# Kernel tuning notes

Measured on AMD Instinct MI355X. Metric: run time of the kernel, lower is better.

## Reference

```python
import jax, jax.numpy as jnp
import numpy as np

LN_EPS = 1e-6

def hsigmoid(v):
    # HSigmoid with bias=3, divisor=6: clamp((v+3)/6, 0, 1)
    return jnp.clip((v + 3.0) / 6.0, 0.0, 1.0)

def setup_inputs() -> dict:
    key = jax.random.key(0)
    ks = jax.random.split(key, 10)
    b, c, h, w = 8, 512, 64, 64
    s = lambda fan: 1.0 / np.sqrt(fan)
    return {
        "x": jax.random.normal(ks[0], (b, c, h, w), jnp.float32),
        "w_b1": jax.random.normal(ks[1], (c // 2, c), jnp.float32) * s(c),
        "b_b1": jax.random.normal(ks[2], (c // 2,), jnp.float32) * 0.01,
        "w_b2": jax.random.normal(ks[3], (c, c // 2), jnp.float32) * s(c // 2),
        "b_b2": jax.random.normal(ks[4], (c,), jnp.float32) * 0.01,
        "w_conv1": jax.random.normal(ks[5], (1, c), jnp.float32) * s(c),
        "ln_g": jnp.ones((c,), jnp.float32),
        "ln_b": jnp.zeros((c,), jnp.float32),
        "sk_w1": jax.random.normal(ks[6], (c // 2, c), jnp.float32) * s(c),
        "sk_w2": jax.random.normal(ks[7], (c, c // 2), jnp.float32) * s(c // 2),
        "res_w": jax.random.normal(ks[8], (c, c), jnp.float32) * s(c),
    }

def reference(x, w_b1, b_b1, w_b2, b_b2, w_conv1, ln_g, ln_b, sk_w1, sk_w2, res_w):
    b, c, h, w = x.shape
    # --- channel attention: GAP -> 1x1 conv+ReLU -> 1x1 conv+HSigmoid -> LN over c ---
    g = x.mean(axis=(2, 3))                                  # (b, c)
    ca = jax.nn.relu(g @ w_b1.T + b_b1)                      # (b, c/2)
    ca = hsigmoid(ca @ w_b2.T + b_b2)                        # (b, c)
    mu = ca.mean(axis=-1, keepdims=True)
    var = ca.var(axis=-1, keepdims=True)
    ca = (ca - mu) / jnp.sqrt(var + LN_EPS) * ln_g + ln_b    # LayerNorm over channels
    channel_attn = ca[:, :, None, None]                      # (b, c, 1, 1)
    # --- spatial attention: 1x1 conv (c->1, no bias) + HSigmoid ---
    spatial_attn = hsigmoid(jnp.einsum('bchw,c->bhw', x, w_conv1[0]))[:, None]  # (b,1,h,w)
    # --- parallel attention: torch float // 2 == floor((a+b)/2) ---
    par_attn = jnp.floor((spatial_attn + channel_attn) / 2.0)  # (b, c, h, w)
    # --- sequence attention: bmm outer product (b,c,1)x(b,1,hw) ---
    seq_attn = channel_attn * spatial_attn                     # (b, c, h, w)
    # --- SK module: GAP(sum) -> conv+ReLU -> conv+ReLU -> softmax over c ---
    u = (seq_attn + par_attn).mean(axis=(2, 3))                # (b, c)
    u = jax.nn.relu(u @ sk_w1.T)
    u = jax.nn.relu(u @ sk_w2.T)
    a = jax.nn.softmax(u, axis=1)[:, :, None, None]            # (b, c, 1, 1)
    selected_attn = seq_attn * a + par_attn * (1.0 - a)        # (b, c, h, w)
    # --- self attention: spatial sum + 1x1 residual conv ---
    self_attn = selected_attn.sum(axis=(2, 3))[:, :, None, None] \
        + jnp.einsum('bchw,oc->bohw', x, res_w)                # (b, c, h, w)
    return x * selected_attn + self_attn
```

## Files before the change

### kernel.cpp

```cpp
#include <hip/hip_runtime.h>
#include <stdint.h>

#define HW 4096
#define NC 512
#define NB 8

typedef __attribute__((ext_vector_type(8))) short short8;
typedef __attribute__((ext_vector_type(4))) float f32x4;

__device__ __forceinline__ unsigned short f2bf(float f) {
  unsigned int u = __builtin_bit_cast(unsigned int, f);
  unsigned int r = (u + 0x7FFFu + ((u >> 16) & 1u)) >> 16;
  return (unsigned short)r;
}
__device__ __forceinline__ float hsig(float v) {
  return fminf(fmaxf((v + 3.0f) * (1.0f / 6.0f), 0.0f), 1.0f);
}

__device__ __forceinline__ void gload16(const void* g, void* l) {
  __builtin_amdgcn_global_load_lds(
      (const __attribute__((address_space(1))) unsigned int*)g,
      (__attribute__((address_space(3))) unsigned int*)l, 16, 0, 0);
}

__device__ __forceinline__ float wave_reduce(float p) {
#pragma unroll
  for (int m = 1; m < 64; m <<= 1) p += __shfl_xor(p, m);
  return p;
}

__device__ __forceinline__ float block_reduce_sum16(float v, volatile float* red) {
  int t = threadIdx.x;
#pragma unroll
  for (int m = 1; m < 64; m <<= 1) v += __shfl_xor(v, m);
  if ((t & 63) == 0) red[t >> 6] = v;
  __syncthreads();
  v = 0.f;
#pragma unroll
  for (int i = 0; i < 16; i++) v += red[i];
  __syncthreads();
  return v;
}
__device__ __forceinline__ float block_reduce_max16(float v, volatile float* red) {
  int t = threadIdx.x;
#pragma unroll
  for (int m = 1; m < 64; m <<= 1) v = fmaxf(v, __shfl_xor(v, m));
  if ((t & 63) == 0) red[t >> 6] = v;
  __syncthreads();
  v = red[0];
#pragma unroll
  for (int i = 1; i < 16; i++) v = fmaxf(v, red[i]);
  __syncthreads();
  return v;
}

__global__ __launch_bounds__(256) void k1_stats_transpose(
    const float* __restrict__ x, const float* __restrict__ w_conv1,
    const float* __restrict__ res_w,
    float* __restrict__ g_sum, float* __restrict__ spat,
    unsigned short* __restrict__ xTS, unsigned short* __restrict__ wbfS) {
  __shared__ float sp_lds[16][64];
  __shared__ unsigned short t_lds[64 * 72];
  const int t = threadIdx.x;
  const int b = blockIdx.z;
  const int c0 = blockIdx.y * 64;
  const int h0 = blockIdx.x * 64;
  const int cg = t >> 4;
  const int hg = t & 15;

  float vv[4][4];
  float wc[4];
  const float* xb = x + ((size_t)(b * NC + c0 + cg * 4) * HW) + h0 + hg * 4;
#pragma unroll
  for (int i = 0; i < 4; i++) {
    float4 v = *(const float4*)(xb + (size_t)i * HW);
    vv[i][0] = v.x; vv[i][1] = v.y; vv[i][2] = v.z; vv[i][3] = v.w;
    wc[i] = w_conv1[c0 + cg * 4 + i];
  }
#pragma unroll
  for (int i = 0; i < 4; i++) {
    float s = vv[i][0] + vv[i][1] + vv[i][2] + vv[i][3];
    s += __shfl_xor(s, 1); s += __shfl_xor(s, 2);
    s += __shfl_xor(s, 4); s += __shfl_xor(s, 8);
    if (hg == 0) atomicAdd(&g_sum[b * NC + c0 + cg * 4 + i], s);
  }
  {
    float4 sp;
    sp.x = vv[0][0] * wc[0] + vv[1][0] * wc[1] + vv[2][0] * wc[2] + vv[3][0] * wc[3];
    sp.y = vv[0][1] * wc[0] + vv[1][1] * wc[1] + vv[2][1] * wc[2] + vv[3][1] * wc[3];
    sp.z = vv[0][2] * wc[0] + vv[1][2] * wc[1] + vv[2][2] * wc[2] + vv[3][2] * wc[3];
    sp.w = vv[0][3] * wc[0] + vv[1][3] * wc[1] + vv[2][3] * wc[2] + vv[3][3] * wc[3];
    *(float4*)&sp_lds[cg][hg * 4] = sp;
  }
#pragma unroll
  for (int j = 0; j < 4; j++) {
    ushort4 u;
    u.x = f2bf(vv[0][j]); u.y = f2bf(vv[1][j]);
    u.z = f2bf(vv[2][j]); u.w = f2bf(vv[3][j]);
    *(ushort4*)&t_lds[(hg * 4 + j) * 72 + cg * 4] = u;
  }
  __syncthreads();
  if (t < 64) {
    float s = 0.f;
#pragma unroll
    for (int i = 0; i < 16; i++) s += sp_lds[i][t];
    atomicAdd(&spat[b * HW + h0 + t], s);
  }
  const int w = t >> 6, l = t & 63;
#pragma unroll
  for (int ff = w; ff < 8; ff += 4) {
    const int fr = ff >> 1, fk = ff & 1;
    short8 v = *(const short8*)&t_lds[(fr * 16 + (l & 15)) * 72 + (fk * 4 + (l >> 4)) * 8];
    size_t tile = (size_t)(b * 256 + (h0 >> 4) + fr) * 16 + (c0 >> 5) + fk;
    *(short8*)(xTS + tile * 512 + l * 8) = v;
  }
  if (b == 0 && t < 64) {
    const int q = blockIdx.y * 64 + blockIdx.x;
    float4 a = *(const float4*)(res_w + (size_t)q * 512 + t * 8);
    float4 c2 = *(const float4*)(res_w + (size_t)q * 512 + t * 8 + 4);
    short8 v;
    v[0] = (short)f2bf(a.x); v[1] = (short)f2bf(a.y);
    v[2] = (short)f2bf(a.z); v[3] = (short)f2bf(a.w);
    v[4] = (short)f2bf(c2.x); v[5] = (short)f2bf(c2.y);
    v[6] = (short)f2bf(c2.z); v[7] = (short)f2bf(c2.w);
    const int lq = (q & 15) + ((t & 3) << 4);
    *(short8*)(wbfS + ((size_t)(q >> 4) * 16 + (t >> 2)) * 512 + lq * 8) = v;
  }
}

__global__ __launch_bounds__(1024) void k2_front(
    const float* __restrict__ g_sum, const float* __restrict__ spat,
    const float* __restrict__ w_b1, const float* __restrict__ b_b1,
    const float* __restrict__ w_b2, const float* __restrict__ b_b2,
    const float* __restrict__ ln_g, const float* __restrict__ ln_b,
    float* __restrict__ s_out, float* __restrict__ Ssum,
    float* __restrict__ t_arr) {
  __shared__ float ca1_l[256];
  __shared__ float ca2_l[512];
  __shared__ float red[16];
  const int b = blockIdx.x, t = threadIdx.x;
  const int w = t >> 6, l = t & 63;

  {
    float4 v = ((const float4*)(spat + (size_t)b * HW))[t];
    float4 os;
    os.x = hsig(v.x); os.y = hsig(v.y); os.z = hsig(v.z); os.w = hsig(v.w);
    ((float4*)(s_out + (size_t)b * HW))[t] = os;
    float Ss = block_reduce_sum16(os.x + os.y + os.z + os.w, red);
    if (t == 0) Ssum[b] = Ss;
  }

  float ga[8];
  {
    const float4 g0 = *(const float4*)(g_sum + b * NC + l * 8);
    const float4 g1 = *(const float4*)(g_sum + b * NC + l * 8 + 4);
    ga[0] = g0.x; ga[1] = g0.y; ga[2] = g0.z; ga[3] = g0.w;
    ga[4] = g1.x; ga[5] = g1.y; ga[6] = g1.z; ga[7] = g1.w;
  }
#pragma unroll
  for (int jj = 0; jj < 4; jj++) {
    float pr[4];
#pragma unroll
    for (int q = 0; q < 4; q++) {
      const int o = w + 16 * (jj * 4 + q);
      const float* wr = w_b1 + (size_t)o * 512 + l * 8;
      float4 wa = *(const float4*)wr;
      float4 wb = *(const float4*)(wr + 4);
      pr[q] = wa.x * ga[0] + wa.y * ga[1] + wa.z * ga[2] + wa.w * ga[3] +
              wb.x * ga[4] + wb.y * ga[5] + wb.z * ga[6] + wb.w * ga[7];
    }
#pragma unroll
    for (int q = 0; q < 4; q++) pr[q] = wave_reduce(pr[q]);
    if (l == 0) {
#pragma unroll
      for (int q = 0; q < 4; q++) {
        const int o = w + 16 * (jj * 4 + q);
        ca1_l[o] = fmaxf(pr[q] * (1.0f / 4096.0f) + b_b1[o], 0.0f);
      }
    }
  }
  __syncthreads();

  {
    float4 c4 = *(float4*)&ca1_l[l * 4];
#pragma unroll
    for (int jj = 0; jj < 8; jj++) {
      float pr[4];
#pragma unroll
      for (int q = 0; q < 4; q++) {
        const int o = w + 16 * (jj * 4 + q);
        float4 wv = ((const float4*)(w_b2 + (size_t)o * 256))[l];
        pr[q] = wv.x * c4.x + wv.y * c4.y + wv.z * c4.z + wv.w * c4.w;
      }
#pragma unroll
      for (int q = 0; q < 4; q++) pr[q] = wave_reduce(pr[q]);
      if (l == 0) {
#pragma unroll
        for (int q = 0; q < 4; q++) {
          const int o = w + 16 * (jj * 4 + q);
          ca2_l[o] = hsig(pr[q] + b_b2[o]);
        }
      }
    }
  }
  __syncthreads();

  {
    float val = (t < 512) ? ca2_l[t] : 0.f;
    float S = block_reduce_sum16(val, red);
    float SQ = block_reduce_sum16(val * val, red);
    float mu = S * (1.0f / 512.0f);
    float var = SQ * (1.0f / 512.0f) - mu * mu;
    float rstd = rsqrtf(var + 1e-6f);
    if (t < 512) t_arr[b * NC + t] = (val - mu) * rstd * ln_g[t] + ln_b[t];
  }
}

__global__ __launch_bounds__(256) void k2b_floorsum(
    const float* __restrict__ s, const float* __restrict__ t_arr, float* __restrict__ P) {
  __shared__ float s_l[4096];
  const int t = threadIdx.x;
  const int b = blockIdx.y;
  const int c0 = blockIdx.x * 16;
  const float* sb = s + b * HW;
#pragma unroll
  for (int i = 0; i < 16; i++) s_l[t + i * 256] = sb[t + i * 256];
  __syncthreads();
  const int w = t >> 6, l = t & 63;
#pragma unroll
  for (int j = 0; j < 4; j++) {
    int c = c0 + w * 4 + j;
    float tc = t_arr[b * NC + c];
    float sum = 0.f;
#pragma unroll 8
    for (int i = 0; i < 64; i++) sum += floorf((s_l[l + i * 64] + tc) * 0.5f);
#pragma unroll
    for (int m = 1; m < 64; m <<= 1) sum += __shfl_xor(sum, m);
    if (l == 0) P[b * NC + c] = sum;
  }
}

__global__ __launch_bounds__(1024) void k2_back(
    const float* __restrict__ t_arr, const float* __restrict__ P,
    const float* __restrict__ Ssum, const float* __restrict__ sk_w1,
    const float* __restrict__ sk_w2, float* __restrict__ coef) {
  __shared__ float u1_l[256];
  __shared__ float u2_l[512];
  __shared__ float red[16];
  const int b = blockIdx.x, t = threadIdx.x;
  const int w = t >> 6, l = t & 63;
  const float Ss = Ssum[b];

  float ua[8];
  {
    const float* tr = t_arr + b * NC + l * 8;
    const float* pr = P + b * NC + l * 8;
    float4 ta = *(const float4*)tr, tb = *(const float4*)(tr + 4);
    float4 Pa = *(const float4*)pr, Pb = *(const float4*)(pr + 4);
    ua[0] = ta.x * Ss + Pa.x; ua[1] = ta.y * Ss + Pa.y;
    ua[2] = ta.z * Ss + Pa.z; ua[3] = ta.w * Ss + Pa.w;
    ua[4] = tb.x * Ss + Pb.x; ua[5] = tb.y * Ss + Pb.y;
    ua[6] = tb.z * Ss + Pb.z; ua[7] = tb.w * Ss + Pb.w;
  }
#pragma unroll
  for (int jj = 0; jj < 4; jj++) {
    float pr[4];
#pragma unroll
    for (int q = 0; q < 4; q++) {
      const int o = w + 16 * (jj * 4 + q);
      const float* wr = sk_w1 + (size_t)o * 512 + l * 8;
      float4 wa = *(const float4*)wr;
      float4 wb = *(const float4*)(wr + 4);
      pr[q] = wa.x * ua[0] + wa.y * ua[1] + wa.z * ua[2] + wa.w * ua[3] +
              wb.x * ua[4] + wb.y * ua[5] + wb.z * ua[6] + wb.w * ua[7];
    }
#pragma unroll
    for (int q = 0; q < 4; q++) pr[q] = wave_reduce(pr[q]) * (1.0f / 4096.0f);
    if (l == 0) {
#pragma unroll
      for (int q = 0; q < 4; q++) {
        const int o = w + 16 * (jj * 4 + q);
        u1_l[o] = fmaxf(pr[q], 0.0f);
      }
    }
  }
  __syncthreads();

  {
    float4 c4 = *(float4*)&u1_l[l * 4];
#pragma unroll
    for (int jj = 0; jj < 8; jj++) {
      float pr[4];
#pragma unroll
      for (int q = 0; q < 4; q++) {
        const int o = w + 16 * (jj * 4 + q);
        float4 wv = ((const float4*)(sk_w2 + (size_t)o * 256))[l];
        pr[q] = wv.x * c4.x + wv.y * c4.y + wv.z * c4.z + wv.w * c4.w;
      }
#pragma unroll
      for (int q = 0; q < 4; q++) pr[q] = wave_reduce(pr[q]);
      if (l == 0) {
#pragma unroll
        for (int q = 0; q < 4; q++) {
          const int o = w + 16 * (jj * 4 + q);
          u2_l[o] = fmaxf(pr[q], 0.0f);
        }
      }
    }
  }
  __syncthreads();

  {
    float val = (t < 512) ? u2_l[t] : -3.402823466e38f;
    float M = block_reduce_max16(val, red);
    float e = (t < 512) ? __expf(val - M) : 0.f;
    float Z = block_reduce_sum16(e, red);
    if (t < 512) {
      float a = e / Z;
      float tc = t_arr[b * NC + t];
      float Pv = P[b * NC + t];
      float c1 = a * tc;
      float c2 = 1.0f - a;
      float c3 = c1 * Ss + c2 * Pv;
      float4 cf = {c1, c2, c3, tc};
      *(float4*)(coef + (size_t)(b * NC + t) * 4) = cf;
    }
  }
}

__global__ __launch_bounds__(256, 4) void k3_gemm_epilogue(
    const unsigned short* __restrict__ wbfS, const unsigned short* __restrict__ xTS,
    const float* __restrict__ x, const float* __restrict__ s,
    const float* __restrict__ coef, float* __restrict__ out) {
  __shared__ __align__(16) char smem[32768];
  const int t = threadIdx.x;
  const int bx = blockIdx.x, mz = blockIdx.y, b = blockIdx.z;
  const int w = t >> 6, l = t & 63;
  const int wm = w >> 1, wn = w & 1;
  const int l16 = l & 15, quad = l >> 4;

  f32x4 acc[4][4];
#pragma unroll
  for (int mi = 0; mi < 4; mi++)
#pragma unroll
    for (int ni = 0; ni < 4; ni++) {
      f32x4 z = {0.f, 0.f, 0.f, 0.f};
      acc[mi][ni] = z;
    }

  const char* gA0 = (const char*)wbfS + ((size_t)(mz * 8 + 2 * w) * 16) * 1024 + l * 16;
  const char* gA1 = gA0 + 16 * 1024;
  const char* gB0 = (const char*)xTS + ((size_t)(b * 256 + bx * 8 + 2 * w) * 16) * 1024 + l * 16;
  const char* gB1 = gB0 + 16 * 1024;
  char* lA0 = smem + (2 * w) * 1024;
  char* lA1 = smem + (2 * w + 1) * 1024;
  char* lB0 = smem + 8192 + (2 * w) * 1024;
  char* lB1 = smem + 8192 + (2 * w + 1) * 1024;
  const char* pA = smem + wm * 4096 + l * 16;
  const char* pB = smem + 8192 + wn * 4096 + l * 16;

#define K3_STAGE(buf, kk) do {                                  \
    gload16(gA0 + (kk) * 1024, lA0 + (buf) * 16384);            \
    gload16(gA1 + (kk) * 1024, lA1 + (buf) * 16384);            \
    gload16(gB0 + (kk) * 1024, lB0 + (buf) * 16384);            \
    gload16(gB1 + (kk) * 1024, lB1 + (buf) * 16384);            \
  } while (0)

#define K3_COMPUTE(buf) do {                                    \
    short8 af[4], bfr[4];                                       \
    _Pragma("unroll")                                           \
    for (int mi = 0; mi < 4; mi++)                              \
      af[mi] = *(const short8*)(pA + (buf) * 16384 + mi * 1024);\
    _Pragma("unroll")                                           \
    for (int ni = 0; ni < 4; ni++)                              \
      bfr[ni] = *(const short8*)(pB + (buf) * 16384 + ni * 1024);\
    _Pragma("unroll")                                           \
    for (int mi = 0; mi < 4; mi++)                              \
      _Pragma("unroll")                                         \
      for (int ni = 0; ni < 4; ni++)                            \
        acc[mi][ni] = __builtin_amdgcn_mfma_f32_16x16x32_bf16(  \
            af[mi], bfr[ni], acc[mi][ni], 0, 0, 0);             \
  } while (0)

  K3_STAGE(0, 0);
  __syncthreads();
#pragma unroll
  for (int kk = 0; kk < 16; kk += 2) {
    K3_STAGE(1, kk + 1);
    K3_COMPUTE(0);
    __syncthreads();
    if (kk + 2 < 16) K3_STAGE(0, kk + 2);
    K3_COMPUTE(1);
    __syncthreads();
  }

  float* eb = (float*)smem + w * 1088;
  const int row = l >> 2, cb = (l & 3) * 16;
  const int colb = bx * 128 + wn * 64 + cb;
  const float* sp = s + b * HW + colb;
  float4 sv[4];
#pragma unroll
  for (int j = 0; j < 4; j++) sv[j] = *(const float4*)(sp + 4 * j);
#pragma unroll
  for (int mi = 0; mi < 4; mi++) {
#pragma unroll
    for (int ni = 0; ni < 4; ni++)
#pragma unroll
      for (int r = 0; r < 4; r++)
        eb[(quad * 4 + r) * 68 + ni * 16 + l16] = acc[mi][ni][r];
    const int o = mz * 128 + wm * 64 + mi * 16 + row;
    float4 cf = *(const float4*)(coef + (size_t)(b * NC + o) * 4);
    const size_t rbase = (size_t)(b * NC + o) * HW + colb;
#pragma unroll
    for (int j = 0; j < 4; j++) {
      f32x4 y = *(f32x4*)&eb[row * 68 + cb + 4 * j];
      float4 svj = sv[j];
      float4 xv = *(const float4*)(x + rbase + 4 * j);
      float4 ov;
      ov.x = xv.x * (cf.x * svj.x + cf.y * floorf((svj.x + cf.w) * 0.5f)) + cf.z + y.x;
      ov.y = xv.y * (cf.x * svj.y + cf.y * floorf((svj.y + cf.w) * 0.5f)) + cf.z + y.y;
      ov.z = xv.z * (cf.x * svj.z + cf.y * floorf((svj.z + cf.w) * 0.5f)) + cf.z + y.z;
      ov.w = xv.w * (cf.x * svj.w + cf.y * floorf((svj.w + cf.w) * 0.5f)) + cf.z + y.w;
      *(float4*)(out + rbase + 4 * j) = ov;
    }
  }
#undef K3_STAGE
#undef K3_COMPUTE
}

extern "C" void kernel_launch(void* const* d_in, const int* in_sizes, int n_in,
                              void* d_out, int out_size, void* d_ws, size_t ws_size,
                              hipStream_t stream) {
  const float* x       = (const float*)d_in[0];
  const float* w_b1    = (const float*)d_in[1];
  const float* b_b1    = (const float*)d_in[2];
  const float* w_b2    = (const float*)d_in[3];
  const float* b_b2    = (const float*)d_in[4];
  const float* w_conv1 = (const float*)d_in[5];
  const float* ln_g    = (const float*)d_in[6];
  const float* ln_b    = (const float*)d_in[7];
  const float* sk_w1   = (const float*)d_in[8];
  const float* sk_w2   = (const float*)d_in[9];
  const float* res_w   = (const float*)d_in[10];
  float* out = (float*)d_out;
  char* ws = (char*)d_ws;

  float* g_sum = (float*)(ws + 0x00000);
  float* spat  = (float*)(ws + 0x08000);
  float* Ssum  = (float*)(ws + 0x28000);
  float* t_arr = (float*)(ws + 0x29000);
  float* P     = (float*)(ws + 0x30000);
  float* coef  = (float*)(ws + 0x38000);
  float* s     = (float*)(ws + 0x50000);
  unsigned short* wbfS = (unsigned short*)(ws + 0x80000);
  unsigned short* xTS  = (unsigned short*)(ws + 0x100000);

  hipMemsetAsync(ws, 0, 0x28000, stream);
  k1_stats_transpose<<<dim3(64, 8, 8), 256, 0, stream>>>(x, w_conv1, res_w, g_sum, spat, xTS, wbfS);
  k2_front<<<8, 1024, 0, stream>>>(g_sum, spat, w_b1, b_b1, w_b2, b_b2, ln_g, ln_b, s, Ssum, t_arr);
  k2b_floorsum<<<dim3(32, 8), 256, 0, stream>>>(s, t_arr, P);
  k2_back<<<8, 1024, 0, stream>>>(t_arr, P, Ssum, sk_w1, sk_w2, coef);
  k3_gemm_epilogue<<<dim3(32, 4, 8), 256, 0, stream>>>(wbfS, xTS, x, s, coef, out);
}
```

Measured before the change: 236.2 us.

## Fuse small middle kernels, spread front/back MLPs over more blocks, move softmax into GEMM

Merges the front MLP/LayerNorm kernel with the floor-sum kernel, so each of 32x8 blocks of 256 threads recomputes the channel MLP and then handles its own 16 channels. The back kernel is split the same way, with each block writing only its slice of u2. The softmax and coefficient computation move into the GEMM prologue, where each block writes them to LDS. This removes one launch and the serial 8-block kernels, but adds redundant MLP work per block and extra prologue latency to every GEMM block.

```diff
diff --git a/kernel.cpp b/kernel.cpp
--- a/kernel.cpp
+++ b/kernel.cpp
@@ -29,27 +29,23 @@
   return p;
 }
 
-__device__ __forceinline__ float block_reduce_sum16(float v, volatile float* red) {
+__device__ __forceinline__ float block_reduce_sum(float v, volatile float* red) {
   int t = threadIdx.x;
 #pragma unroll
   for (int m = 1; m < 64; m <<= 1) v += __shfl_xor(v, m);
   if ((t & 63) == 0) red[t >> 6] = v;
   __syncthreads();
-  v = 0.f;
-#pragma unroll
-  for (int i = 0; i < 16; i++) v += red[i];
+  v = red[0] + red[1] + red[2] + red[3];
   __syncthreads();
   return v;
 }
-__device__ __forceinline__ float block_reduce_max16(float v, volatile float* red) {
+__device__ __forceinline__ float block_reduce_max(float v, volatile float* red) {
   int t = threadIdx.x;
 #pragma unroll
   for (int m = 1; m < 64; m <<= 1) v = fmaxf(v, __shfl_xor(v, m));
   if ((t & 63) == 0) red[t >> 6] = v;
   __syncthreads();
-  v = red[0];
-#pragma unroll
-  for (int i = 1; i < 16; i++) v = fmaxf(v, red[i]);
+  v = fmaxf(fmaxf(red[0], red[1]), fmaxf(red[2], red[3]));
   __syncthreads();
   return v;
 }
@@ -128,25 +124,34 @@
   }
 }
 
-__global__ __launch_bounds__(1024) void k2_front(
+__global__ __launch_bounds__(256) void k2x_front(
     const float* __restrict__ g_sum, const float* __restrict__ spat,
     const float* __restrict__ w_b1, const float* __restrict__ b_b1,
     const float* __restrict__ w_b2, const float* __restrict__ b_b2,
     const float* __restrict__ ln_g, const float* __restrict__ ln_b,
     float* __restrict__ s_out, float* __restrict__ Ssum,
-    float* __restrict__ t_arr) {
+    float* __restrict__ t_arr, float* __restrict__ P) {
+  __shared__ float s_l[4096];
   __shared__ float ca1_l[256];
   __shared__ float ca2_l[512];
-  __shared__ float red[16];
-  const int b = blockIdx.x, t = threadIdx.x;
+  __shared__ float red[4];
+  const int t = threadIdx.x;
+  const int bx = blockIdx.x, b = blockIdx.y;
   const int w = t >> 6, l = t & 63;
 
-  {
-    float4 v = ((const float4*)(spat + (size_t)b * HW))[t];
-    float4 os;
-    os.x = hsig(v.x); os.y = hsig(v.y); os.z = hsig(v.z); os.w = hsig(v.w);
-    ((float4*)(s_out + (size_t)b * HW))[t] = os;
-    float Ss = block_reduce_sum16(os.x + os.y + os.z + os.w, red);
+#pragma unroll
+  for (int i = 0; i < 16; i++)
+    s_l[t + i * 256] = hsig(spat[(size_t)b * HW + t + i * 256]);
+  __syncthreads();
+  if (t < 32) {
+    float4 v = ((const float4*)(s_l + bx * 128))[t];
+    ((float4*)(s_out + (size_t)b * HW + bx * 128))[t] = v;
+  }
+  if (bx == 0) {
+    float part = 0.f;
+#pragma unroll
+    for (int i = 0; i < 16; i++) part += s_l[t + i * 256];
+    float Ss = block_reduce_sum(part, red);
     if (t == 0) Ssum[b] = Ss;
   }
 
@@ -157,12 +162,12 @@
     ga[0] = g0.x; ga[1] = g0.y; ga[2] = g0.z; ga[3] = g0.w;
     ga[4] = g1.x; ga[5] = g1.y; ga[6] = g1.z; ga[7] = g1.w;
   }
-#pragma unroll
-  for (int jj = 0; jj < 4; jj++) {
+#pragma unroll 2
+  for (int rr = 0; rr < 64; rr += 4) {
     float pr[4];
 #pragma unroll
     for (int q = 0; q < 4; q++) {
-      const int o = w + 16 * (jj * 4 + q);
+      const int o = (rr + q) * 4 + w;
       const float* wr = w_b1 + (size_t)o * 512 + l * 8;
       float4 wa = *(const float4*)wr;
       float4 wb = *(const float4*)(wr + 4);
@@ -174,7 +179,7 @@
     if (l == 0) {
 #pragma unroll
       for (int q = 0; q < 4; q++) {
-        const int o = w + 16 * (jj * 4 + q);
+        const int o = (rr + q) * 4 + w;
         ca1_l[o] = fmaxf(pr[q] * (1.0f / 4096.0f) + b_b1[o], 0.0f);
       }
     }
@@ -183,12 +188,12 @@
 
   {
     float4 c4 = *(float4*)&ca1_l[l * 4];
-#pragma unroll
-    for (int jj = 0; jj < 8; jj++) {
+#pragma unroll 2
+    for (int rr = 0; rr < 128; rr += 4) {
       float pr[4];
 #pragma unroll
       for (int q = 0; q < 4; q++) {
-        const int o = w + 16 * (jj * 4 + q);
+        const int o = (rr + q) * 4 + w;
         float4 wv = ((const float4*)(w_b2 + (size_t)o * 256))[l];
         pr[q] = wv.x * c4.x + wv.y * c4.y + wv.z * c4.z + wv.w * c4.w;
       }
@@ -197,7 +202,7 @@
       if (l == 0) {
 #pragma unroll
         for (int q = 0; q < 4; q++) {
-          const int o = w + 16 * (jj * 4 + q);
+          const int o = (rr + q) * 4 + w;
           ca2_l[o] = hsig(pr[q] + b_b2[o]);
         }
       }
@@ -205,32 +210,19 @@
   }
   __syncthreads();
 
-  {
-    float val = (t < 512) ? ca2_l[t] : 0.f;
-    float S = block_reduce_sum16(val, red);
-    float SQ = block_reduce_sum16(val * val, red);
-    float mu = S * (1.0f / 512.0f);
-    float var = SQ * (1.0f / 512.0f) - mu * mu;
-    float rstd = rsqrtf(var + 1e-6f);
-    if (t < 512) t_arr[b * NC + t] = (val - mu) * rstd * ln_g[t] + ln_b[t];
-  }
-}
-
-__global__ __launch_bounds__(256) void k2b_floorsum(
-    const float* __restrict__ s, const float* __restrict__ t_arr, float* __restrict__ P) {
-  __shared__ float s_l[4096];
-  const int t = threadIdx.x;
-  const int b = blockIdx.y;
-  const int c0 = blockIdx.x * 16;
-  const float* sb = s + b * HW;
-#pragma unroll
-  for (int i = 0; i < 16; i++) s_l[t + i * 256] = sb[t + i * 256];
-  __syncthreads();
-  const int w = t >> 6, l = t & 63;
+  float v0 = ca2_l[t], v1 = ca2_l[t + 256];
+  float S = block_reduce_sum(v0 + v1, red);
+  float SQ = block_reduce_sum(v0 * v0 + v1 * v1, red);
+  float mu = S * (1.0f / 512.0f);
+  float var = SQ * (1.0f / 512.0f) - mu * mu;
+  float rstd = rsqrtf(var + 1e-6f);
+
+  const int c0 = bx * 16;
 #pragma unroll
   for (int j = 0; j < 4; j++) {
     int c = c0 + w * 4 + j;
-    float tc = t_arr[b * NC + c];
+    float tc = (ca2_l[c] - mu) * rstd * ln_g[c] + ln_b[c];
+    if (l == 0) t_arr[b * NC + c] = tc;
     float sum = 0.f;
 #pragma unroll 8
     for (int i = 0; i < 64; i++) sum += floorf((s_l[l + i * 64] + tc) * 0.5f);
@@ -240,14 +232,13 @@
   }
 }
 
-__global__ __launch_bounds__(1024) void k2_back(
+__global__ __launch_bounds__(256) void k2y_back(
     const float* __restrict__ t_arr, const float* __restrict__ P,
     const float* __restrict__ Ssum, const float* __restrict__ sk_w1,
-    const float* __restrict__ sk_w2, float* __restrict__ coef) {
+    const float* __restrict__ sk_w2, float* __restrict__ u2) {
   __shared__ float u1_l[256];
-  __shared__ float u2_l[512];
-  __shared__ float red[16];
-  const int b = blockIdx.x, t = threadIdx.x;
+  const int t = threadIdx.x;
+  const int bx = blockIdx.x, b = blockIdx.y;
   const int w = t >> 6, l = t & 63;
   const float Ss = Ssum[b];
 
@@ -262,12 +253,12 @@
     ua[4] = tb.x * Ss + Pb.x; ua[5] = tb.y * Ss + Pb.y;
     ua[6] = tb.z * Ss + Pb.z; ua[7] = tb.w * Ss + Pb.w;
   }
-#pragma unroll
-  for (int jj = 0; jj < 4; jj++) {
+#pragma unroll 2
+  for (int rr = 0; rr < 64; rr += 4) {
     float pr[4];
 #pragma unroll
     for (int q = 0; q < 4; q++) {
-      const int o = w + 16 * (jj * 4 + q);
+      const int o = (rr + q) * 4 + w;
       const float* wr = sk_w1 + (size_t)o * 512 + l * 8;
       float4 wa = *(const float4*)wr;
       float4 wb = *(const float4*)(wr + 4);
@@ -279,7 +270,7 @@
     if (l == 0) {
 #pragma unroll
       for (int q = 0; q < 4; q++) {
-        const int o = w + 16 * (jj * 4 + q);
+        const int o = (rr + q) * 4 + w;
         u1_l[o] = fmaxf(pr[q], 0.0f);
       }
     }
@@ -288,42 +279,21 @@
 
   {
     float4 c4 = *(float4*)&u1_l[l * 4];
-#pragma unroll
-    for (int jj = 0; jj < 8; jj++) {
-      float pr[4];
+    float pr[4];
+#pragma unroll
+    for (int q = 0; q < 4; q++) {
+      const int o = bx * 16 + q * 4 + w;
+      float4 wv = ((const float4*)(sk_w2 + (size_t)o * 256))[l];
+      pr[q] = wv.x * c4.x + wv.y * c4.y + wv.z * c4.z + wv.w * c4.w;
+    }
+#pragma unroll
+    for (int q = 0; q < 4; q++) pr[q] = wave_reduce(pr[q]);
+    if (l == 0) {
 #pragma unroll
       for (int q = 0; q < 4; q++) {
-        const int o = w + 16 * (jj * 4 + q);
-        float4 wv = ((const float4*)(sk_w2 + (size_t)o * 256))[l];
-        pr[q] = wv.x * c4.x + wv.y * c4.y + wv.z * c4.z + wv.w * c4.w;
+        const int o = bx * 16 + q * 4 + w;
+        u2[b * NC + o] = fmaxf(pr[q], 0.0f);
       }
-#pragma unroll
-      for (int q = 0; q < 4; q++) pr[q] = wave_reduce(pr[q]);
-      if (l == 0) {
-#pragma unroll
-        for (int q = 0; q < 4; q++) {
-          const int o = w + 16 * (jj * 4 + q);
-          u2_l[o] = fmaxf(pr[q], 0.0f);
-        }
-      }
-    }
-  }
-  __syncthreads();
-
-  {
-    float val = (t < 512) ? u2_l[t] : -3.402823466e38f;
-    float M = block_reduce_max16(val, red);
-    float e = (t < 512) ? __expf(val - M) : 0.f;
-    float Z = block_reduce_sum16(e, red);
-    if (t < 512) {
-      float a = e / Z;
-      float tc = t_arr[b * NC + t];
-      float Pv = P[b * NC + t];
-      float c1 = a * tc;
-      float c2 = 1.0f - a;
-      float c3 = c1 * Ss + c2 * Pv;
-      float4 cf = {c1, c2, c3, tc};
-      *(float4*)(coef + (size_t)(b * NC + t) * 4) = cf;
     }
   }
 }
@@ -331,13 +301,37 @@
 __global__ __launch_bounds__(256, 4) void k3_gemm_epilogue(
     const unsigned short* __restrict__ wbfS, const unsigned short* __restrict__ xTS,
     const float* __restrict__ x, const float* __restrict__ s,
-    const float* __restrict__ coef, float* __restrict__ out) {
-  __shared__ __align__(16) char smem[32768];
+    const float* __restrict__ u2, const float* __restrict__ t_arr,
+    const float* __restrict__ P, const float* __restrict__ Ssum,
+    float* __restrict__ out) {
+  __shared__ __align__(16) char smem[34816];
+  __shared__ float red4[4];
   const int t = threadIdx.x;
   const int bx = blockIdx.x, mz = blockIdx.y, b = blockIdx.z;
   const int w = t >> 6, l = t & 63;
   const int wm = w >> 1, wn = w & 1;
   const int l16 = l & 15, quad = l >> 4;
+
+  float4* cf_l = (float4*)(smem + 32768);
+  {
+    const float Ss = Ssum[b];
+    float v0 = u2[b * NC + t], v1 = u2[b * NC + t + 256];
+    float M = block_reduce_max(fmaxf(v0, v1), red4);
+    float e0 = __expf(v0 - M), e1 = __expf(v1 - M);
+    float Z = block_reduce_sum(e0 + e1, red4);
+    float inv = 1.0f / Z;
+    if (t < 128) {
+      const int o = mz * 128 + t;
+      float a = __expf(u2[b * NC + o] - M) * inv;
+      float tc = t_arr[b * NC + o];
+      float Pv = P[b * NC + o];
+      float c1 = a * tc;
+      float c2v = 1.0f - a;
+      float c3 = c1 * Ss + c2v * Pv;
+      float4 cf = {c1, c2v, c3, tc};
+      cf_l[t] = cf;
+    }
+  }
 
   f32x4 acc[4][4];
 #pragma unroll
@@ -409,7 +403,7 @@
       for (int r = 0; r < 4; r++)
         eb[(quad * 4 + r) * 68 + ni * 16 + l16] = acc[mi][ni][r];
     const int o = mz * 128 + wm * 64 + mi * 16 + row;
-    float4 cf = *(const float4*)(coef + (size_t)(b * NC + o) * 4);
+    float4 cf = cf_l[wm * 64 + mi * 16 + row];
     const size_t rbase = (size_t)(b * NC + o) * HW + colb;
 #pragma unroll
     for (int j = 0; j < 4; j++) {
@@ -450,15 +444,14 @@
   float* Ssum  = (float*)(ws + 0x28000);
   float* t_arr = (float*)(ws + 0x29000);
   float* P     = (float*)(ws + 0x30000);
-  float* coef  = (float*)(ws + 0x38000);
   float* s     = (float*)(ws + 0x50000);
+  float* u2    = (float*)(ws + 0x78000);
   unsigned short* wbfS = (unsigned short*)(ws + 0x80000);
   unsigned short* xTS  = (unsigned short*)(ws + 0x100000);
 
   hipMemsetAsync(ws, 0, 0x28000, stream);
   k1_stats_transpose<<<dim3(64, 8, 8), 256, 0, stream>>>(x, w_conv1, res_w, g_sum, spat, xTS, wbfS);
-  k2_front<<<8, 1024, 0, stream>>>(g_sum, spat, w_b1, b_b1, w_b2, b_b2, ln_g, ln_b, s, Ssum, t_arr);
-  k2b_floorsum<<<dim3(32, 8), 256, 0, stream>>>(s, t_arr, P);
-  k2_back<<<8, 1024, 0, stream>>>(t_arr, P, Ssum, sk_w1, sk_w2, coef);
-  k3_gemm_epilogue<<<dim3(32, 4, 8), 256, 0, stream>>>(wbfS, xTS, x, s, coef, out);
-}
+  k2x_front<<<dim3(32, 8), 256, 0, stream>>>(g_sum, spat, w_b1, b_b1, w_b2, b_b2, ln_g, ln_b, s, Ssum, t_arr, P);
+  k2y_back<<<dim3(32, 8), 256, 0, stream>>>(t_arr, P, Ssum, sk_w1, sk_w2, u2);
+  k3_gemm_epilogue<<<dim3(32, 4, 8), 256, 0, stream>>>(wbfS, xTS, x, s, u2, t_arr, P, Ssum, out);
+}
```

New measurement: 264.8 us. 1.12x slower.
